# Kernel tuning notes

Measured on AMD Instinct MI355X. Metric: run time of the kernel, lower is better.

## Reference

```python
import jax, jax.numpy as jnp
import numpy as np

B, C, U = 8, 32, 32
K = 5            # powers = k + 1 with k = 4
N1, N2 = 256, 256


def setup_inputs() -> dict:
    key = jax.random.key(0)
    k_x, k_c1, k_c2, k_w = jax.random.split(key, 4)
    x = jax.random.normal(k_x, (B, C, N1, N2), dtype=jnp.float32)
    # Chebyshev polynomial bases T_0..T_k of the (rescaled) Laplacians of the
    # two factor graphs; registered buffers in the torch module.
    cheb1 = jax.random.normal(k_c1, (K, N1, N1), dtype=jnp.float32)
    cheb2 = jax.random.normal(k_c2, (K, N2, N2), dtype=jnp.float32)
    # Trainable anisotropic coefficients [powers, powers, channels, units],
    # initialized N(0, 0.001) in the original module.
    coefs = jax.random.normal(k_w, (K, K, C, U), dtype=jnp.float32) * 0.001
    return {"x": x, "cheb1": cheb1, "cheb2": cheb2, "coefs": coefs}


def reference(x, cheb1, cheb2, coefs):
    """Fused form of the anisotropic Chebyshev convolution.

    Original triple loop computes
      out[b,u,m,n] = sum_{k1,k2,i,p,q}
          coefs[k1,k2,i,u] * cheb1[k1,p,m] * cheb2[k2,q,n] * x[b,i,p,q]
    """
    # Filter along the first graph axis for every power k1: [B, K, C, N1, N2]
    a = jnp.einsum('kpm,bipq->bkimq', cheb1, x)
    # Contract channels and k1 with the learned coefficients: [B, K, U, N1, N2]
    c = jnp.einsum('bkimq,kliu->blumq', a, coefs)
    # Filter along the second graph axis for every power k2: [B, U, N1, N2]
    out = jnp.einsum('blumq,lqn->bumn', c, cheb2)
    return out
```

## Files before the change

### kernel.cpp

```cpp
#include <hip/hip_runtime.h>
#include <stdint.h>

#define WB 8
#define WC 32
#define WU 32
#define WK 5
#define WN 256
#define NN 65536
#define KC 160
#define KQ 1280

typedef __attribute__((ext_vector_type(8))) short bf8;
typedef __attribute__((ext_vector_type(8))) unsigned short us8;
typedef __attribute__((ext_vector_type(4))) float f4;

__device__ __forceinline__ unsigned short f2b(float f) {
    union { float f; uint32_t u; } v; v.f = f;
    uint32_t u = v.u;
    return (unsigned short)((u + 0x7FFFu + ((u >> 16) & 1u)) >> 16);
}

__device__ __forceinline__ void gload16(const unsigned short* g, unsigned short* l) {
    __builtin_amdgcn_global_load_lds(
        (const __attribute__((address_space(1))) unsigned int*)g,
        (__attribute__((address_space(3))) unsigned int*)l, 16, 0, 0);
}

__global__ void prep_small(const float* __restrict__ cheb1,
                           const float* __restrict__ cheb2,
                           const float* __restrict__ coefs,
                           unsigned short* __restrict__ c1T,
                           unsigned short* __restrict__ c2T,
                           unsigned short* __restrict__ WtP) {
    int idx = blockIdx.x * 256 + threadIdx.x;
    if (idx < WK * NN) {
        int k = idx / NN, r = idx % NN, m = r / WN, p = r % WN;
        c1T[idx] = f2b(cheb1[(k * WN + p) * WN + m]);
    }
    if (idx < WN * KQ) {
        int n = idx / KQ, r = idx % KQ;
        c2T[idx] = f2b(cheb2[r * WN + n]);
    }
    if (idx < KC * KC) {
        int e = idx & 7, lane = (idx >> 3) & 63, r = idx >> 9;
        int mf = r % 5, kk = (r / 5) % 5, mh = r / 25;
        int lu = mh * 80 + mf * 16 + (lane & 15);
        int ki = kk * 32 + (lane >> 4) * 8 + e;
        int l = lu >> 5, u = lu & 31, k = ki >> 5, i = ki & 31;
        WtP[idx] = f2b(coefs[((k * WK + l) * WC + i) * WU + u]);
    }
}

__global__ void prep_x(const float* __restrict__ x, unsigned short* __restrict__ xT) {
    __shared__ unsigned short tile[64][72];
    int bi = blockIdx.z;
    int p0 = blockIdx.y * 64, q0 = blockIdx.x * 64;
    const float* src = x + (size_t)bi * NN;
    unsigned short* dst = xT + (size_t)bi * NN;
    int t = threadIdx.x;
    int c4 = (t & 15) * 4, r0 = t >> 4;
    for (int it = 0; it < 4; ++it) {
        int r = r0 + it * 16;
        float4 v = *reinterpret_cast<const float4*>(&src[(size_t)(p0 + r) * WN + q0 + c4]);
        tile[r][c4 + 0] = f2b(v.x); tile[r][c4 + 1] = f2b(v.y);
        tile[r][c4 + 2] = f2b(v.z); tile[r][c4 + 3] = f2b(v.w);
    }
    __syncthreads();
    for (int it = 0; it < 4; ++it) {
        int q = r0 + it * 16;
        ushort4 o;
        o.x = tile[c4 + 0][q]; o.y = tile[c4 + 1][q];
        o.z = tile[c4 + 2][q]; o.w = tile[c4 + 3][q];
        *reinterpret_cast<ushort4*>(&dst[(size_t)(q0 + q) * WN + p0 + c4]) = o;
    }
}

__global__ __launch_bounds__(512, 4) void g1(const unsigned short* __restrict__ c1T,
                                             const unsigned short* __restrict__ xT,
                                             unsigned short* __restrict__ a, int b_base) {
    __shared__ unsigned short As[2][128 * 64];
    __shared__ unsigned short Bs[256 * 64];
    int p = blockIdx.x;
    int gpx = gridDim.x / 80;
    int xcd = p & 7, j = p >> 3;
    int grp = xcd * gpx + j / 10;
    int member = j % 10;
    int bl = grp >> 5, i = grp & 31;
    int row0 = member * 128;
    int b = b_base + bl;
    const unsigned short* Asrc = c1T;
    const unsigned short* Bsrc = xT + (size_t)(b * WC + i) * NN;
    unsigned short* Out = a + (size_t)bl * KC * NN;

    int t = threadIdx.x;
    int w = t >> 6, l = t & 63;
    int wm = (w >> 2) * 64, wn = (w & 3) * 64;
    int lr = l & 15, hi = l >> 4;
    int srow = l >> 3;
    int scol = ((l & 7) ^ srow) * 8;

    f4 acc[4][4];
    for (int mf = 0; mf < 4; ++mf) for (int nf = 0; nf < 4; ++nf) acc[mf][nf] = (f4)(0.0f);

#define G1_STAGE_A(buf, step) do { \
    int p0_ = (step) * 64; \
    for (int it = 0; it < 2; ++it) { \
        int chunk = it * 8 + w; int row = chunk * 8 + srow; \
        gload16(&Asrc[(size_t)(row0 + row) * 256 + p0_ + scol], &As[buf][chunk * 512]); } \
} while (0)
#define G1_STAGE_B(step) do { \
    int p0_ = (step) * 64; \
    for (int it = 0; it < 4; ++it) { \
        int chunk = it * 8 + w; int row = chunk * 8 + srow; \
        gload16(&Bsrc[(size_t)row * 256 + p0_ + scol], &Bs[chunk * 512]); } \
} while (0)

    G1_STAGE_A(0, 0);
    for (int step = 0; step < 4; ++step) {
        int cur = step & 1;
        G1_STAGE_B(step);
        if (step < 3) {
            G1_STAGE_A(cur ^ 1, step + 1);
            asm volatile("s_waitcnt vmcnt(2)" ::: "memory");
        } else {
            asm volatile("s_waitcnt vmcnt(0)" ::: "memory");
        }
        __builtin_amdgcn_s_barrier();
        asm volatile("" ::: "memory");
        for (int kk = 0; kk < 2; ++kk) {
            bf8 af[4], bfr[4];
            for (int mf = 0; mf < 4; ++mf) {
                int r = wm + mf * 16 + lr;
                af[mf] = *(const bf8*)&As[cur][r * 64 + (((kk * 4 + hi) ^ (r & 7)) * 8)];
            }
            for (int nf = 0; nf < 4; ++nf) {
                int rb = wn + nf * 16 + lr;
                bfr[nf] = *(const bf8*)&Bs[rb * 64 + (((kk * 4 + hi) ^ (rb & 7)) * 8)];
            }
            for (int mf = 0; mf < 4; ++mf)
                for (int nf = 0; nf < 4; ++nf)
                    acc[mf][nf] = __builtin_amdgcn_mfma_f32_16x16x32_bf16(af[mf], bfr[nf], acc[mf][nf], 0, 0, 0);
        }
        asm volatile("" ::: "memory");
        __builtin_amdgcn_s_barrier();
    }
#undef G1_STAGE_A
#undef G1_STAGE_B
    for (int mf = 0; mf < 4; ++mf)
        for (int nf = 0; nf < 4; ++nf)
            for (int j2 = 0; j2 < 4; ++j2) {
                int grow = row0 + wm + mf * 16 + hi * 4 + j2;
                int k = grow >> 8, m = grow & 255;
                int q = wn + nf * 16 + lr;
                Out[(size_t)(k * 32 + i) * NN + m * 256 + q] = f2b(acc[mf][nf][j2]);
            }
}

__global__ __launch_bounds__(512, 4) void g2p(const unsigned short* __restrict__ WtP,
                                              const unsigned short* __restrict__ a,
                                              unsigned short* __restrict__ c) {
    __shared__ unsigned short Bt[128 * 172];
    int bl = blockIdx.y;
    int n0 = blockIdx.x * 128;
    const unsigned short* asrc = a + (size_t)bl * KC * NN;
    unsigned short* Out = c + (size_t)bl * KC * NN;
    int t = threadIdx.x;

    for (int s = 0; s < 2; ++s) {
        int task = t + s * 512;
        if (task < 640) {
            int oct = task & 15, kq = task >> 4;
            const unsigned short* src = asrc + (size_t)(kq * 4) * NN + n0 + oct * 8;
            us8 v0 = *(const us8*)&src[0 * NN];
            us8 v1 = *(const us8*)&src[1 * NN];
            us8 v2 = *(const us8*)&src[2 * NN];
            us8 v3 = *(const us8*)&src[3 * NN];
            #pragma unroll
            for (int j = 0; j < 8; ++j) {
                ushort4 wv;
                wv.x = v0[j]; wv.y = v1[j]; wv.z = v2[j]; wv.w = v3[j];
                *reinterpret_cast<ushort4*>(&Bt[(oct * 8 + j) * 172 + kq * 4]) = wv;
            }
        }
    }
    __syncthreads();

    int w = t >> 6, l = t & 63;
    int mh = w >> 2, nq = w & 3;
    int lr = l & 15, hi = l >> 4;
    f4 acc[5][2];
    for (int mf = 0; mf < 5; ++mf) { acc[mf][0] = (f4)(0.0f); acc[mf][1] = (f4)(0.0f); }

    for (int kk = 0; kk < 5; ++kk) {
        int k0 = kk * 32 + hi * 8;
        bf8 bfr[2];
        #pragma unroll
        for (int nf = 0; nf < 2; ++nf) {
            int pix = (nq * 2 + nf) * 16 + lr;
            typedef __attribute__((ext_vector_type(4))) short s4v;
            s4v lo  = *(const s4v*)&Bt[pix * 172 + k0];
            s4v hi4 = *(const s4v*)&Bt[pix * 172 + k0 + 4];
            bfr[nf] = __builtin_shufflevector(lo, hi4, 0, 1, 2, 3, 4, 5, 6, 7);
        }
        #pragma unroll
        for (int mf = 0; mf < 5; ++mf) {
            bf8 afr = *(const bf8*)&WtP[(size_t)((((mh * 5 + kk) * 5 + mf) << 6) + l) * 8];
            acc[mf][0] = __builtin_amdgcn_mfma_f32_16x16x32_bf16(afr, bfr[0], acc[mf][0], 0, 0, 0);
            acc[mf][1] = __builtin_amdgcn_mfma_f32_16x16x32_bf16(afr, bfr[1], acc[mf][1], 0, 0, 0);
        }
    }
    for (int mf = 0; mf < 5; ++mf)
        for (int nf = 0; nf < 2; ++nf)
            for (int j = 0; j < 4; ++j) {
                int row = mh * 80 + mf * 16 + hi * 4 + j;
                int col = n0 + (nq * 2 + nf) * 16 + lr;
                Out[(size_t)row * NN + col] = f2b(acc[mf][nf][j]);
            }
}

__global__ __launch_bounds__(512, 4) void g3(const unsigned short* __restrict__ c,
                                             const unsigned short* __restrict__ c2T,
                                             float* __restrict__ out, int b_base) {
    __shared__ unsigned short As[2][128 * 64];
    __shared__ unsigned short Bs[256 * 64];
    int bl = blockIdx.y;
    int b = b_base + bl;
    int R0 = blockIdx.x * 128;
    int u = R0 >> 8, m0 = R0 & 255;
    const unsigned short* Csrc = c + (size_t)bl * KC * NN;

    int t = threadIdx.x;
    int w = t >> 6, l = t & 63;
    int wm = (w >> 2) * 64, wn = (w & 3) * 64;
    int lr = l & 15, hi = l >> 4;
    int srow = l >> 3;
    int scol = ((l & 7) ^ srow) * 8;

    f4 acc[4][4];
    for (int mf = 0; mf < 4; ++mf) for (int nf = 0; nf < 4; ++nf) acc[mf][nf] = (f4)(0.0f);

#define G3_STAGE_A(buf, step) do { \
    int lq_ = (step) >> 2, q0_ = ((step) & 3) * 64; \
    const unsigned short* Arow0 = Csrc + (size_t)(lq_ * 32 + u) * NN + (size_t)m0 * 256 + q0_; \
    for (int it = 0; it < 2; ++it) { \
        int chunk = it * 8 + w; int row = chunk * 8 + srow; \
        gload16(&Arow0[(size_t)row * 256 + scol], &As[buf][chunk * 512]); } \
} while (0)
#define G3_STAGE_B(step) do { \
    const unsigned short* Brow0 = c2T + (step) * 64; \
    for (int it = 0; it < 4; ++it) { \
        int chunk = it * 8 + w; int row = chunk * 8 + srow; \
        gload16(&Brow0[(size_t)row * KQ + scol], &Bs[chunk * 512]); } \
} while (0)

    G3_STAGE_A(0, 0);
    for (int step = 0; step < 20; ++step) {
        int cur = step & 1;
        G3_STAGE_B(step);
        if (step < 19) {
            G3_STAGE_A(cur ^ 1, step + 1);
            asm volatile("s_waitcnt vmcnt(2)" ::: "memory");
        } else {
            asm volatile("s_waitcnt vmcnt(0)" ::: "memory");
        }
        __builtin_amdgcn_s_barrier();
        asm volatile("" ::: "memory");
        for (int kk = 0; kk < 2; ++kk) {
            bf8 af[4], bfr[4];
            for (int mf = 0; mf < 4; ++mf) {
                int r = wm + mf * 16 + lr;
                af[mf] = *(const bf8*)&As[cur][r * 64 + (((kk * 4 + hi) ^ (r & 7)) * 8)];
            }
            for (int nf = 0; nf < 4; ++nf) {
                int rb = wn + nf * 16 + lr;
                bfr[nf] = *(const bf8*)&Bs[rb * 64 + (((kk * 4 + hi) ^ (rb & 7)) * 8)];
            }
            for (int mf = 0; mf < 4; ++mf)
                for (int nf = 0; nf < 4; ++nf)
                    acc[mf][nf] = __builtin_amdgcn_mfma_f32_16x16x32_bf16(af[mf], bfr[nf], acc[mf][nf], 0, 0, 0);
        }
        asm volatile("" ::: "memory");
        __builtin_amdgcn_s_barrier();
    }
#undef G3_STAGE_A
#undef G3_STAGE_B
    for (int mf = 0; mf < 4; ++mf)
        for (int nf = 0; nf < 4; ++nf)
            for (int j = 0; j < 4; ++j) {
                int m = m0 + wm + mf * 16 + hi * 4 + j;
                int n = wn + nf * 16 + lr;
                out[((size_t)(b * WU + u) * WN + m) * WN + n] = acc[mf][nf][j];
            }
}

extern "C" void kernel_launch(void* const* d_in, const int* in_sizes, int n_in,
                              void* d_out, int out_size, void* d_ws, size_t ws_size,
                              hipStream_t stream) {
    const float* x     = (const float*)d_in[0];
    const float* cheb1 = (const float*)d_in[1];
    const float* cheb2 = (const float*)d_in[2];
    const float* coefs = (const float*)d_in[3];
    float* out = (float*)d_out;
    unsigned short* ws = (unsigned short*)d_ws;

    size_t off = 0;
    unsigned short* xT  = ws + off; off += (size_t)WB * WC * NN;
    unsigned short* c1T = ws + off; off += (size_t)WK * NN;
    unsigned short* c2T = ws + off; off += (size_t)WN * KQ;
    unsigned short* WtP = ws + off; off += (size_t)KC * KC;
    size_t fixed_elems = off;
    size_t a1 = (size_t)KC * NN;

    prep_small<<<1280, 256, 0, stream>>>(cheb1, cheb2, coefs, c1T, c2T, WtP);
    prep_x<<<dim3(4, 4, WB * WC), 256, 0, stream>>>(x, xT);

    size_t avail = ws_size / 2;
    size_t rem = avail > fixed_elems ? avail - fixed_elems : 0;

    if (rem >= 9 * a1) {
        int nb = (int)((rem - 8 * a1) / a1);
        if (nb < 1) nb = 1;
        if (nb > WB) nb = WB;
        unsigned short* a_ = ws + fixed_elems;
        unsigned short* c_ = a_ + (size_t)nb * a1;
        for (int b0 = 0; b0 < WB; b0 += nb) {
            int cur = (WB - b0 < nb) ? (WB - b0) : nb;
            g1<<<dim3(cur * 320), 512, 0, stream>>>(c1T, xT, a_, b0);
            g2p<<<dim3(512, cur), 512, 0, stream>>>(WtP, a_, c_ + (size_t)b0 * a1);
        }
        g3<<<dim3(64, WB), 512, 0, stream>>>(c_, c2T, out, 0);
    } else {
        size_t per_b = 2 * a1;
        int nb = (int)(rem / per_b);
        if (nb < 1) nb = 1;
        if (nb > WB) nb = WB;
        unsigned short* a_ = ws + fixed_elems;
        unsigned short* c_ = a_ + (size_t)nb * a1;
        for (int b0 = 0; b0 < WB; b0 += nb) {
            int cur = (WB - b0 < nb) ? (WB - b0) : nb;
            g1<<<dim3(cur * 320), 512, 0, stream>>>(c1T, xT, a_, b0);
            g2p<<<dim3(512, cur), 512, 0, stream>>>(WtP, a_, c_);
            g3<<<dim3(64, cur), 512, 0, stream>>>(c_, c2T, out, b0);
        }
    }
}
```

Before: 262.8 us.

## Enlarge g3 tile to 256x256 with double-buffered A/B and interleaved loads

The final GEMM kernel g3 now computes a full 256x256 output tile per block (one block per batch/unit) instead of 128x256, doubling per-wave accumulators to 8x4 fragments. Both A and B tiles are double-buffered in LDS, and next-stage global-to-LDS loads are spread between MFMA groups with s_setprio raised around the MFMA bursts. This reuses each B tile across more rows and cuts barriers per step. In exchange, the grid halves to 256 blocks, occupancy drops to one block per CU, and LDS use grows to 128 KB.

```diff
diff --git a/kernel.cpp b/kernel.cpp
--- a/kernel.cpp
+++ b/kernel.cpp
@@ -218,76 +218,108 @@
             }
 }
 
-__global__ __launch_bounds__(512, 4) void g3(const unsigned short* __restrict__ c,
+__global__ __launch_bounds__(512, 1) void g3(const unsigned short* __restrict__ c,
                                              const unsigned short* __restrict__ c2T,
                                              float* __restrict__ out, int b_base) {
-    __shared__ unsigned short As[2][128 * 64];
-    __shared__ unsigned short Bs[256 * 64];
+    __shared__ unsigned short As[2][256 * 64];
+    __shared__ unsigned short Bs[2][256 * 64];
     int bl = blockIdx.y;
     int b = b_base + bl;
-    int R0 = blockIdx.x * 128;
-    int u = R0 >> 8, m0 = R0 & 255;
+    int u = blockIdx.x;
     const unsigned short* Csrc = c + (size_t)bl * KC * NN;
 
-    int t = threadIdx.x;
-    int w = t >> 6, l = t & 63;
-    int wm = (w >> 2) * 64, wn = (w & 3) * 64;
+    int t_ = threadIdx.x;
+    int w = t_ >> 6, l = t_ & 63;
+    int wm = (w >> 2) * 128, wn = (w & 3) * 64;
     int lr = l & 15, hi = l >> 4;
     int srow = l >> 3;
     int scol = ((l & 7) ^ srow) * 8;
 
-    f4 acc[4][4];
-    for (int mf = 0; mf < 4; ++mf) for (int nf = 0; nf < 4; ++nf) acc[mf][nf] = (f4)(0.0f);
-
-#define G3_STAGE_A(buf, step) do { \
-    int lq_ = (step) >> 2, q0_ = ((step) & 3) * 64; \
-    const unsigned short* Arow0 = Csrc + (size_t)(lq_ * 32 + u) * NN + (size_t)m0 * 256 + q0_; \
+    f4 acc[8][4];
+    for (int mf = 0; mf < 8; ++mf) for (int nf = 0; nf < 4; ++nf) acc[mf][nf] = (f4)(0.0f);
+
+#define ST_A(s, h, kt) do { \
+    int lq_ = (kt) >> 2, q0_ = ((kt) & 3) * 64; \
+    const unsigned short* base = Csrc + (size_t)(lq_ * 32 + u) * NN + q0_; \
     for (int it = 0; it < 2; ++it) { \
-        int chunk = it * 8 + w; int row = chunk * 8 + srow; \
-        gload16(&Arow0[(size_t)row * 256 + scol], &As[buf][chunk * 512]); } \
+        int chunk = it * 8 + w; int row = (h) * 128 + chunk * 8 + srow; \
+        gload16(&base[(size_t)row * 256 + scol], &As[s][(h) * 8192 + chunk * 512]); } \
 } while (0)
-#define G3_STAGE_B(step) do { \
-    const unsigned short* Brow0 = c2T + (step) * 64; \
-    for (int it = 0; it < 4; ++it) { \
-        int chunk = it * 8 + w; int row = chunk * 8 + srow; \
-        gload16(&Brow0[(size_t)row * KQ + scol], &Bs[chunk * 512]); } \
+#define ST_B(s, h, kt) do { \
+    const unsigned short* base = c2T + (size_t)((h) * 128) * KQ + (kt) * 64; \
+    for (int it = 0; it < 2; ++it) { \
+        int chunk = it * 8 + w; int rrow = chunk * 8 + srow; \
+        gload16(&base[(size_t)rrow * KQ + scol], &Bs[s][(h) * 8192 + chunk * 512]); } \
 } while (0)
 
-    G3_STAGE_A(0, 0);
-    for (int step = 0; step < 20; ++step) {
-        int cur = step & 1;
-        G3_STAGE_B(step);
-        if (step < 19) {
-            G3_STAGE_A(cur ^ 1, step + 1);
-            asm volatile("s_waitcnt vmcnt(2)" ::: "memory");
-        } else {
-            asm volatile("s_waitcnt vmcnt(0)" ::: "memory");
-        }
+    ST_A(0, 0, 0); ST_A(0, 1, 0); ST_B(0, 0, 0); ST_B(0, 1, 0);
+
+    for (int t = 0; t < 20; ++t) {
+        int s = t & 1;
+        asm volatile("s_waitcnt vmcnt(0)" ::: "memory");
         __builtin_amdgcn_s_barrier();
         asm volatile("" ::: "memory");
-        for (int kk = 0; kk < 2; ++kk) {
-            bf8 af[4], bfr[4];
-            for (int mf = 0; mf < 4; ++mf) {
-                int r = wm + mf * 16 + lr;
-                af[mf] = *(const bf8*)&As[cur][r * 64 + (((kk * 4 + hi) ^ (r & 7)) * 8)];
-            }
-            for (int nf = 0; nf < 4; ++nf) {
-                int rb = wn + nf * 16 + lr;
-                bfr[nf] = *(const bf8*)&Bs[rb * 64 + (((kk * 4 + hi) ^ (rb & 7)) * 8)];
-            }
-            for (int mf = 0; mf < 4; ++mf)
-                for (int nf = 0; nf < 4; ++nf)
-                    acc[mf][nf] = __builtin_amdgcn_mfma_f32_16x16x32_bf16(af[mf], bfr[nf], acc[mf][nf], 0, 0, 0);
-        }
+        const unsigned short* A = As[s];
+        const unsigned short* B = Bs[s];
+        bf8 af[8], b0, b1;
+        if (t < 19) ST_A(s ^ 1, 0, t + 1);
+        #pragma unroll
+        for (int mf = 0; mf < 8; ++mf) {
+            int r = wm + mf * 16 + lr;
+            af[mf] = *(const bf8*)&A[r * 64 + ((hi ^ (r & 7)) * 8)];
+        }
+        { int rb = wn + lr;      b0 = *(const bf8*)&B[rb * 64 + ((hi ^ (rb & 7)) * 8)];
+          rb = wn + 16 + lr;     b1 = *(const bf8*)&B[rb * 64 + ((hi ^ (rb & 7)) * 8)]; }
+        __builtin_amdgcn_s_setprio(1);
+        #pragma unroll
+        for (int mf = 0; mf < 8; ++mf) {
+            acc[mf][0] = __builtin_amdgcn_mfma_f32_16x16x32_bf16(af[mf], b0, acc[mf][0], 0, 0, 0);
+            acc[mf][1] = __builtin_amdgcn_mfma_f32_16x16x32_bf16(af[mf], b1, acc[mf][1], 0, 0, 0);
+        }
+        __builtin_amdgcn_s_setprio(0);
+        if (t < 19) ST_A(s ^ 1, 1, t + 1);
+        { int rb = wn + 32 + lr; b0 = *(const bf8*)&B[rb * 64 + ((hi ^ (rb & 7)) * 8)];
+          rb = wn + 48 + lr;     b1 = *(const bf8*)&B[rb * 64 + ((hi ^ (rb & 7)) * 8)]; }
+        __builtin_amdgcn_s_setprio(1);
+        #pragma unroll
+        for (int mf = 0; mf < 8; ++mf) {
+            acc[mf][2] = __builtin_amdgcn_mfma_f32_16x16x32_bf16(af[mf], b0, acc[mf][2], 0, 0, 0);
+            acc[mf][3] = __builtin_amdgcn_mfma_f32_16x16x32_bf16(af[mf], b1, acc[mf][3], 0, 0, 0);
+        }
+        __builtin_amdgcn_s_setprio(0);
+        if (t < 19) ST_B(s ^ 1, 0, t + 1);
+        #pragma unroll
+        for (int mf = 0; mf < 8; ++mf) {
+            int r = wm + mf * 16 + lr;
+            af[mf] = *(const bf8*)&A[r * 64 + (((4 + hi) ^ (r & 7)) * 8)];
+        }
+        { int rb = wn + lr;      b0 = *(const bf8*)&B[rb * 64 + (((4 + hi) ^ (rb & 7)) * 8)];
+          rb = wn + 16 + lr;     b1 = *(const bf8*)&B[rb * 64 + (((4 + hi) ^ (rb & 7)) * 8)]; }
+        __builtin_amdgcn_s_setprio(1);
+        #pragma unroll
+        for (int mf = 0; mf < 8; ++mf) {
+            acc[mf][0] = __builtin_amdgcn_mfma_f32_16x16x32_bf16(af[mf], b0, acc[mf][0], 0, 0, 0);
+            acc[mf][1] = __builtin_amdgcn_mfma_f32_16x16x32_bf16(af[mf], b1, acc[mf][1], 0, 0, 0);
+        }
+        __builtin_amdgcn_s_setprio(0);
+        if (t < 19) ST_B(s ^ 1, 1, t + 1);
+        { int rb = wn + 32 + lr; b0 = *(const bf8*)&B[rb * 64 + (((4 + hi) ^ (rb & 7)) * 8)];
+          rb = wn + 48 + lr;     b1 = *(const bf8*)&B[rb * 64 + (((4 + hi) ^ (rb & 7)) * 8)]; }
+        __builtin_amdgcn_s_setprio(1);
+        #pragma unroll
+        for (int mf = 0; mf < 8; ++mf) {
+            acc[mf][2] = __builtin_amdgcn_mfma_f32_16x16x32_bf16(af[mf], b0, acc[mf][2], 0, 0, 0);
+            acc[mf][3] = __builtin_amdgcn_mfma_f32_16x16x32_bf16(af[mf], b1, acc[mf][3], 0, 0, 0);
+        }
+        __builtin_amdgcn_s_setprio(0);
         asm volatile("" ::: "memory");
-        __builtin_amdgcn_s_barrier();
-    }
-#undef G3_STAGE_A
-#undef G3_STAGE_B
-    for (int mf = 0; mf < 4; ++mf)
+    }
+#undef ST_A
+#undef ST_B
+    for (int mf = 0; mf < 8; ++mf)
         for (int nf = 0; nf < 4; ++nf)
             for (int j = 0; j < 4; ++j) {
-                int m = m0 + wm + mf * 16 + hi * 4 + j;
+                int m = wm + mf * 16 + hi * 4 + j;
                 int n = wn + nf * 16 + lr;
                 out[((size_t)(b * WU + u) * WN + m) * WN + n] = acc[mf][nf][j];
             }
@@ -328,7 +360,7 @@
             g1<<<dim3(cur * 320), 512, 0, stream>>>(c1T, xT, a_, b0);
             g2p<<<dim3(512, cur), 512, 0, stream>>>(WtP, a_, c_ + (size_t)b0 * a1);
         }
-        g3<<<dim3(64, WB), 512, 0, stream>>>(c_, c2T, out, 0);
+        g3<<<dim3(32, WB), 512, 0, stream>>>(c_, c2T, out, 0);
     } else {
         size_t per_b = 2 * a1;
         int nb = (int)(rem / per_b);
@@ -340,7 +372,7 @@
             int cur = (WB - b0 < nb) ? (WB - b0) : nb;
             g1<<<dim3(cur * 320), 512, 0, stream>>>(c1T, xT, a_, b0);
             g2p<<<dim3(512, cur), 512, 0, stream>>>(WtP, a_, c_);
-            g3<<<dim3(64, cur), 512, 0, stream>>>(c_, c2T, out, b0);
-        }
-    }
-}
+            g3<<<dim3(32, cur), 512, 0, stream>>>(c_, c2T, out, b0);
+        }
+    }
+}
```

After: 269.9 us. +2.7%, slower.
